# Kernel tuning notes

Hardware: AMD Instinct MI355X
Metric: run time of the kernel (lower is better)

The kernel has to match this reference:

```python
import jax, jax.numpy as jnp
import numpy as np

N = 16384      # total points
B = 8          # point clouds in batch
PER = N // B   # points per cloud (batch ids sorted in blocks)
M = 4096       # sampled centers (ratio 0.25, strided sampler -> batch-aligned)
K = 64         # max_num_neighbors
R = 0.25       # ball-query radius
C_IN = 128
HID = 256
C_OUT = 256


def setup_inputs() -> dict:
    key = jax.random.key(0)
    k1, k2, k3, k4, k5 = jax.random.split(key, 5)
    x = jax.random.normal(k1, (N, C_IN), dtype=jnp.float32)
    pos = jax.random.uniform(k2, (N, 3), dtype=jnp.float32)  # unit cube
    batch = jnp.repeat(jnp.arange(B, dtype=jnp.int32), PER)  # sorted block batch ids
    lframes = jax.random.normal(k3, (N, 3, 3), dtype=jnp.float32)
    W1 = jax.random.normal(k4, (2 * C_IN + 3, HID), dtype=jnp.float32) * 0.05
    b1 = jnp.zeros((HID,), dtype=jnp.float32)
    W2 = jax.random.normal(k5, (HID, C_OUT), dtype=jnp.float32) * 0.05
    b2 = jnp.zeros((C_OUT,), dtype=jnp.float32)
    return {"x": x, "pos": pos, "batch": batch, "lframes": lframes,
            "W1": W1, "b1": b1, "W2": W2, "b2": b2}


def _ball_query(pos, batch, idx):
    """radius(pos, pos[idx], R, batch, batch[idx], max_num_neighbors=K).
    Returns fixed-size neighbor indices [M, K] + validity mask [M, K]."""
    pos_c = pos[idx]                                  # [M, 3]
    # squared distances via gemm trick (avoid [M, N, 3] broadcast)
    d2 = ((pos_c ** 2).sum(-1)[:, None]
          + (pos ** 2).sum(-1)[None, :]
          - 2.0 * pos_c @ pos.T)                      # [M, N]
    valid = (d2 <= R * R) & (batch[idx][:, None] == batch[None, :])
    score = jnp.where(valid, -d2, -jnp.inf)
    vals, nbr = jax.lax.top_k(score, K)               # K nearest within ball
    return nbr, jnp.isfinite(vals)


def reference(x, pos, batch, lframes, W1, b1, W2, b2):
    # center sampler: strided subsample (batch-aligned since batch is block-sorted)
    idx = jnp.arange(0, N, N // M)                    # [M]
    nbr, vmask = _ball_query(pos, batch, idx)         # [M, K]

    pos_dst = pos[idx]                                # [M, 3]
    x_dst = x[idx]                                    # [M, C_IN]
    lframes_dst = lframes[idx]                        # [M, 3, 3]

    # EdgeConv: per-edge message MLP([x_src, x_dst, lframe_dst @ (pos_src - pos_dst)])
    rel = pos[nbr] - pos_dst[:, None, :]              # [M, K, 3]
    rel_loc = jnp.einsum('mij,mkj->mki', lframes_dst, rel)  # rotate into dst frame
    feats = jnp.concatenate([
        x[nbr],                                        # [M, K, C_IN]
        jnp.broadcast_to(x_dst[:, None, :], (M, K, C_IN)),
        rel_loc,
    ], axis=-1)                                        # [M, K, 2*C_IN+3]

    h = jax.nn.relu(feats @ W1 + b1)                   # [M, K, HID]
    msg = h @ W2 + b2                                  # [M, K, C_OUT]

    # masked max aggregation over valid neighbors
    msg = jnp.where(vmask[..., None], msg, -jnp.inf)
    out = msg.max(axis=1)                              # [M, C_OUT]
    out = jnp.where(jnp.isfinite(out), out, 0.0)
    return out, pos_dst, batch[idx], lframes_dst
```

## Files before the change

kernel.cpp:

```cpp
#include <hip/hip_runtime.h>
#include <hip/hip_bf16.h>

#define N_PTS 16384
#define PER   2048
#define M_CTR 4096
#define KNB   64
#define C_IN  128
#define HID   256
#define C_OUT 256

typedef unsigned short u16;
typedef unsigned int u32;
typedef __attribute__((ext_vector_type(8))) short s8v;
typedef __attribute__((ext_vector_type(4))) float f4v;
typedef __attribute__((ext_vector_type(4))) unsigned int u4v;

static __device__ __forceinline__ u16 f2bf(float f) {
    union { float f; unsigned int i; } v; v.f = f;
    unsigned int r = v.i + 0x7FFFu + ((v.i >> 16) & 1u);
    return (u16)(r >> 16);
}

__global__ __launch_bounds__(256) void ballq_kernel(
        const float* __restrict__ pos, int* __restrict__ nbr, int* __restrict__ cnt,
        const float* __restrict__ W1, const float* __restrict__ W2,
        u16* __restrict__ W1aT, u16* __restrict__ W1bT, u16* __restrict__ W2T) {
    __shared__ float cd2[1024];
    __shared__ int   cidx[1024];
    __shared__ int   s_n;
    int m = blockIdx.x, tid = threadIdx.x;

    if (m < 256) {
        int gid = m * 256 + tid;
        int cc = gid >> 8, k = gid & 255;
        W2T[gid] = f2bf(W2[k * 256 + cc]);
        if (gid < 32768) {
            int c1 = gid >> 7, k1 = gid & 127;
            W1aT[gid] = f2bf(W1[k1 * 256 + c1]);
            W1bT[gid] = f2bf(W1[(k1 + 128) * 256 + c1]);
        }
    }

    int c = m * 4;
    int base = (m >> 9) << 11;
    int ln = tid & 63;
    if (tid == 0) s_n = 0;
    __syncthreads();
    float cx = pos[c * 3 + 0], cy = pos[c * 3 + 1], cz = pos[c * 3 + 2];
    float A = __fadd_rn(__fadd_rn(__fmul_rn(cx, cx), __fmul_rn(cy, cy)), __fmul_rn(cz, cz));
    float c2x = __fmul_rn(2.0f, cx);
    float c2y = __fmul_rn(2.0f, cy);
    float c2z = __fmul_rn(2.0f, cz);
    for (int s = 0; s < 8; ++s) {
        int j = base + tid + (s << 8);
        float px = pos[j * 3 + 0], py = pos[j * 3 + 1], pz = pos[j * 3 + 2];
        float B = __fadd_rn(__fadd_rn(__fmul_rn(px, px), __fmul_rn(py, py)), __fmul_rn(pz, pz));
        float C = __fmaf_rn(c2z, pz, __fmaf_rn(c2y, py, __fmul_rn(c2x, px)));
        float d2 = __fsub_rn(__fadd_rn(A, B), C);
        bool hit = (d2 <= 0.0625f);
        unsigned long long mk = __ballot(hit);
        int nb = __popcll(mk & ((1ull << ln) - 1ull));
        int tot = __popcll(mk);
        int bidx = 0;
        if (ln == 0 && tot) bidx = atomicAdd(&s_n, tot);
        bidx = __shfl(bidx, 0, 64);
        if (hit) {
            int a = bidx + nb;
            if (a < 1024) { cd2[a] = d2; cidx[a] = j; }
        }
    }
    __syncthreads();
    int V = s_n < 1024 ? s_n : 1024;
    if (V <= KNB) {
        if (tid < KNB) nbr[m * KNB + tid] = (tid < V) ? cidx[tid] : c;
        if (tid == 0) cnt[m] = V;
    } else {
        for (int e = tid; e < V; e += 256) {
            float de = cd2[e]; int ie = cidx[e];
            int rank = 0;
            for (int q = 0; q < V; ++q) {
                float dq = cd2[q];
                rank += (dq < de) || (dq == de && cidx[q] < ie);
            }
            if (rank < KNB) nbr[m * KNB + rank] = cidx[e];
        }
        if (tid == 0) cnt[m] = KNB;
    }
}

__global__ __launch_bounds__(256) void gemm_xw_kernel(
        const float* __restrict__ x, const u16* __restrict__ W1aT, const u16* __restrict__ W1bT,
        const float* __restrict__ b1, u16* __restrict__ u_out, float* __restrict__ v_out) {
    __shared__ u16 x_lds[64 * 136];
    int blk = blockIdx.x, tid = threadIdx.x;
    int mode = blk >= 256 ? 1 : 0;
    int bb = mode ? blk - 256 : blk;
    const u16* WT = mode ? W1bT : W1aT;
    {
        int r = tid >> 2, q = tid & 3;
        int xrow = bb * 64 + r;
        if (mode) xrow *= 4;
        const float* xp = x + xrow * C_IN + q * 32;
        u16* dst = x_lds + r * 136 + q * 32;
        for (int i = 0; i < 8; ++i) {
            f4v f = *(const f4v*)(xp + i * 4);
            dst[i * 4 + 0] = f2bf(f[0]);
            dst[i * 4 + 1] = f2bf(f[1]);
            dst[i * 4 + 2] = f2bf(f[2]);
            dst[i * 4 + 3] = f2bf(f[3]);
        }
    }
    __syncthreads();
    int lane = tid & 63, w = tid >> 6;
    int quad = lane >> 4, l16 = lane & 15;
    int cb = w * 64;
    f4v acc[4][4] = {};
    for (int k0 = 0; k0 < 128; k0 += 32) {
        s8v a[4], b[4];
        for (int rt = 0; rt < 4; ++rt)
            a[rt] = *(const s8v*)&x_lds[(rt * 16 + l16) * 136 + k0 + quad * 8];
        for (int ct = 0; ct < 4; ++ct)
            b[ct] = *(const s8v*)(WT + (cb + ct * 16 + l16) * 128 + k0 + quad * 8);
        for (int rt = 0; rt < 4; ++rt)
            for (int ct = 0; ct < 4; ++ct)
                acc[rt][ct] = __builtin_amdgcn_mfma_f32_16x16x32_bf16(a[rt], b[ct], acc[rt][ct], 0, 0, 0);
    }
    for (int rt = 0; rt < 4; ++rt)
        for (int ct = 0; ct < 4; ++ct)
            for (int g = 0; g < 4; ++g) {
                int row = rt * 16 + quad * 4 + g;
                int col = cb + ct * 16 + l16;
                float val = acc[rt][ct][g];
                int orow = bb * 64 + row;
                if (mode == 0) u_out[orow * 256 + col] = f2bf(val);
                else           v_out[orow * 256 + col] = val + b1[col];
            }
}

__global__ __launch_bounds__(512, 2) void edge_kernel(
        const u16* __restrict__ u, const float* __restrict__ v,
        const u16* __restrict__ W2T, const float* __restrict__ W1,
        const float* __restrict__ b2, const float* __restrict__ pos,
        const float* __restrict__ lframes, const int* __restrict__ batch,
        const int* __restrict__ nbrg, const int* __restrict__ cnt,
        float* __restrict__ out0, float* __restrict__ out_pos,
        float* __restrict__ out_batch, float* __restrict__ out_lf) {
    __shared__ u16   h_lds[2][128 * 264];
    __shared__ float v_lds[4][2][256];
    __shared__ float w1c_lds[768];
    __shared__ f4v   relc_lds[4][2][64];
    __shared__ u16   nbr_lds[4][2][64];

    int blk = blockIdx.x, tid = threadIdx.x;
    int m0 = ((blk & 7) << 9) | ((blk >> 3) << 3);

    int lane = tid & 63, w = tid >> 6;
    int quad = lane >> 4, l16 = lane & 15;
    int cb = (w & 3) * 64;
    int rbase = (w >> 2) * 64;
    int gsel = w >> 2;

    s8v bfrag[6][4];
    #pragma unroll
    for (int k0 = 0; k0 < 6; ++k0)
        #pragma unroll
        for (int ct = 0; ct < 4; ++ct)
            bfrag[k0][ct] = *(const s8v*)(W2T + (cb + ct * 16 + l16) * 256 + k0 * 32 + quad * 8);

    for (int i = tid; i < 768; i += 512) w1c_lds[i] = W1[65536 + i];
    {
        int pr = tid >> 7, g = (tid >> 6) & 1, t = tid & 63;
        int mm = m0 + pr * 2 + g, cc = mm * 4;
        int j = nbrg[mm * KNB + t];
        nbr_lds[pr][g][t] = (u16)j;
        float rx = pos[j * 3 + 0] - pos[cc * 3 + 0];
        float ry = pos[j * 3 + 1] - pos[cc * 3 + 1];
        float rz = pos[j * 3 + 2] - pos[cc * 3 + 2];
        const float* lf = lframes + cc * 9;
        f4v r;
        r[0] = lf[0] * rx + lf[1] * ry + lf[2] * rz;
        r[1] = lf[3] * rx + lf[4] * ry + lf[5] * rz;
        r[2] = lf[6] * rx + lf[7] * ry + lf[8] * rz;
        r[3] = 0.0f;
        relc_lds[pr][g][t] = r;
    }
    ((f4v*)v_lds)[tid] = *(const f4v*)(v + m0 * 256 + tid * 4);
    if (tid >= 256 && tid < 384) {
        int g = (tid - 256) >> 4, t = tid & 15;
        int mm = m0 + g, cc = mm * 4;
        if (t < 3)            out_pos[mm * 3 + t] = pos[cc * 3 + t];
        else if (t == 3)      out_batch[mm] = (float)batch[cc];
        else if (t < 13)      out_lf[mm * 9 + (t - 4)] = lframes[cc * 9 + (t - 4)];
    }

    int co = (tid & 31) * 8;
    int rs = tid >> 5;

    u4v ug[8];
    #pragma unroll
    for (int g = 0; g < 2; ++g)
        #pragma unroll
        for (int i2 = 0; i2 < 4; ++i2) {
            int rl = rs + i2 * 16;
            int j = nbrg[(m0 + g) * KNB + rl];
            ug[g * 4 + i2] = *(const u4v*)(u + j * 256 + co);
        }
    __syncthreads();

    for (int p = 0; p < 4; ++p) {
        int pb = p & 1;
        int cvp = cnt[m0 + p * 2 + gsel];
        #pragma unroll
        for (int g = 0; g < 2; ++g) {
            f4v vq0 = *(const f4v*)&v_lds[p][g][co];
            f4v vq1 = *(const f4v*)&v_lds[p][g][co + 4];
            f4v wa0 = *(const f4v*)&w1c_lds[co],       wa1 = *(const f4v*)&w1c_lds[co + 4];
            f4v wb0 = *(const f4v*)&w1c_lds[256 + co], wb1 = *(const f4v*)&w1c_lds[256 + co + 4];
            f4v wc0 = *(const f4v*)&w1c_lds[512 + co], wc1 = *(const f4v*)&w1c_lds[512 + co + 4];
            #pragma unroll
            for (int i2 = 0; i2 < 4; ++i2) {
                int rl = rs + i2 * 16;
                int row = g * 64 + rl;
                u4v uu = ug[g * 4 + i2];
                f4v r = relc_lds[p][g][rl];
                float p8[8];
                #pragma unroll
                for (int e = 0; e < 8; ++e) {
                    u32 bits = (e & 1) ? (uu[e >> 1] & 0xFFFF0000u) : (uu[e >> 1] << 16);
                    float va = (e < 4) ? vq0[e] : vq1[e - 4];
                    float a0 = (e < 4) ? wa0[e] : wa1[e - 4];
                    float b0 = (e < 4) ? wb0[e] : wb1[e - 4];
                    float c0 = (e < 4) ? wc0[e] : wc1[e - 4];
                    float pre = fmaf(r[0], a0, fmaf(r[1], b0, fmaf(r[2], c0,
                                  va + __uint_as_float(bits))));
                    p8[e] = fmaxf(pre, 0.0f);
                }
                u4v pk;
                #pragma unroll
                for (int d = 0; d < 4; ++d)
                    pk[d] = __builtin_amdgcn_perm(__float_as_uint(p8[2 * d + 1]),
                                                  __float_as_uint(p8[2 * d]), 0x07060302u);
                *(u4v*)&h_lds[pb][row * 264 + co] = pk;
            }
        }
        __syncthreads();

        if (p < 3) {
            #pragma unroll
            for (int g = 0; g < 2; ++g)
                #pragma unroll
                for (int i2 = 0; i2 < 4; ++i2) {
                    int rl = rs + i2 * 16;
                    int j = (int)nbr_lds[p + 1][g][rl];
                    ug[g * 4 + i2] = *(const u4v*)(u + j * 256 + co);
                }
        }

        s8v bs[2][4];
        #pragma unroll
        for (int kk = 0; kk < 2; ++kk)
            #pragma unroll
            for (int ct = 0; ct < 4; ++ct)
                bs[kk][ct] = *(const s8v*)(W2T + (cb + ct * 16 + l16) * 256 + (6 + kk) * 32 + quad * 8);
        f4v acc[4][4] = {};
        #pragma unroll
        for (int k0 = 0; k0 < 6; ++k0) {
            s8v a[4];
            #pragma unroll
            for (int rt = 0; rt < 4; ++rt)
                a[rt] = *(const s8v*)&h_lds[pb][(rbase + rt * 16 + l16) * 264 + k0 * 32 + quad * 8];
            #pragma unroll
            for (int rt = 0; rt < 4; ++rt)
                #pragma unroll
                for (int ct = 0; ct < 4; ++ct)
                    acc[rt][ct] = __builtin_amdgcn_mfma_f32_16x16x32_bf16(a[rt], bfrag[k0][ct], acc[rt][ct], 0, 0, 0);
        }
        #pragma unroll
        for (int kk = 0; kk < 2; ++kk) {
            int k0 = 6 + kk;
            s8v a[4];
            #pragma unroll
            for (int rt = 0; rt < 4; ++rt)
                a[rt] = *(const s8v*)&h_lds[pb][(rbase + rt * 16 + l16) * 264 + k0 * 32 + quad * 8];
            #pragma unroll
            for (int rt = 0; rt < 4; ++rt)
                #pragma unroll
                for (int ct = 0; ct < 4; ++ct)
                    acc[rt][ct] = __builtin_amdgcn_mfma_f32_16x16x32_bf16(a[rt], bs[kk][ct], acc[rt][ct], 0, 0, 0);
        }
        int mout = m0 + p * 2 + gsel;
        #pragma unroll
        for (int ct = 0; ct < 4; ++ct) {
            float mx = -__builtin_inff();
            #pragma unroll
            for (int rt = 0; rt < 4; ++rt)
                #pragma unroll
                for (int g = 0; g < 4; ++g) {
                    int row = rt * 16 + quad * 4 + g;
                    float val = acc[rt][ct][g];
                    if (row < cvp) mx = fmaxf(mx, val);
                }
            mx = fmaxf(mx, __shfl_xor(mx, 16, 64));
            mx = fmaxf(mx, __shfl_xor(mx, 32, 64));
            if (lane < 16)
                out0[mout * 256 + cb + ct * 16 + l16] = mx + b2[cb + ct * 16 + l16];
        }
    }
}

extern "C" void kernel_launch(void* const* d_in, const int* in_sizes, int n_in,
                              void* d_out, int out_size, void* d_ws, size_t ws_size,
                              hipStream_t stream) {
    const float* x       = (const float*)d_in[0];
    const float* pos     = (const float*)d_in[1];
    const int*   batch   = (const int*)d_in[2];
    const float* lframes = (const float*)d_in[3];
    const float* W1      = (const float*)d_in[4];
    const float* b1      = (const float*)d_in[5];
    const float* W2      = (const float*)d_in[6];
    const float* b2      = (const float*)d_in[7];

    float* out       = (float*)d_out;
    float* out_pos   = out + M_CTR * 256;
    float* out_batch = out_pos + M_CTR * 3;
    float* out_lf    = out_batch + M_CTR;

    char* ws = (char*)d_ws;
    u16*   u_ws = (u16*)(ws);
    float* v_ws = (float*)(ws + 8388608);
    u16*   W1aT = (u16*)(ws + 12582912);
    u16*   W1bT = (u16*)(ws + 12648448);
    u16*   W2T  = (u16*)(ws + 12713984);
    int*   nbr  = (int*)(ws + 12845056);
    int*   cntp = (int*)(ws + 13893632);

    hipLaunchKernelGGL(ballq_kernel, dim3(M_CTR), dim3(256), 0, stream,
                       pos, nbr, cntp, W1, W2, W1aT, W1bT, W2T);
    hipLaunchKernelGGL(gemm_xw_kernel, dim3(320), dim3(256), 0, stream,
                       x, W1aT, W1bT, b1, u_ws, v_ws);
    hipLaunchKernelGGL(edge_kernel, dim3(512), dim3(512), 0, stream,
                       u_ws, v_ws, W2T, W1, b2, pos, lframes, batch, nbr, cntp,
                       out, out_pos, out_batch, out_lf);
}
```

Baseline: 179.6 us.

## Shrink edge kernel LDS footprint to one center per step for higher occupancy

The edge kernel now processes one center per iteration instead of two. Each wave computes 32 output columns instead of 64, and a single 64-row h buffer replaces the double-buffered 128-row buffers. The v tile moves out of LDS and is loaded straight from global memory, and the explicit register prefetch of the next neighbor features is removed. Together these cut per-block LDS use by roughly four times and register pressure, and launch bounds now request 4 blocks. The aim is to hide gather latency with more resident waves. The cost is an extra barrier per iteration, the loss of software prefetch overlap, and twice as many loop iterations with smaller MFMA tiles.

```diff
diff --git a/kernel.cpp b/kernel.cpp
--- a/kernel.cpp
+++ b/kernel.cpp
@@ -137,7 +137,7 @@
             }
 }
 
-__global__ __launch_bounds__(512, 2) void edge_kernel(
+__global__ __launch_bounds__(512, 4) void edge_kernel(
         const u16* __restrict__ u, const float* __restrict__ v,
         const u16* __restrict__ W2T, const float* __restrict__ W1,
         const float* __restrict__ b2, const float* __restrict__ pos,
@@ -145,34 +145,31 @@
         const int* __restrict__ nbrg, const int* __restrict__ cnt,
         float* __restrict__ out0, float* __restrict__ out_pos,
         float* __restrict__ out_batch, float* __restrict__ out_lf) {
-    __shared__ u16   h_lds[2][128 * 264];
-    __shared__ float v_lds[4][2][256];
+    __shared__ u16   h_lds[64 * 264];
     __shared__ float w1c_lds[768];
-    __shared__ f4v   relc_lds[4][2][64];
-    __shared__ u16   nbr_lds[4][2][64];
+    __shared__ f4v   relc_lds[8][64];
+    __shared__ u16   nbr_lds[8][64];
 
     int blk = blockIdx.x, tid = threadIdx.x;
     int m0 = ((blk & 7) << 9) | ((blk >> 3) << 3);
 
     int lane = tid & 63, w = tid >> 6;
     int quad = lane >> 4, l16 = lane & 15;
-    int cb = (w & 3) * 64;
-    int rbase = (w >> 2) * 64;
-    int gsel = w >> 2;
-
-    s8v bfrag[6][4];
+    int cb = w * 32;
+
+    s8v bfrag[4][2];
     #pragma unroll
-    for (int k0 = 0; k0 < 6; ++k0)
-        #pragma unroll
-        for (int ct = 0; ct < 4; ++ct)
+    for (int k0 = 0; k0 < 4; ++k0)
+        #pragma unroll
+        for (int ct = 0; ct < 2; ++ct)
             bfrag[k0][ct] = *(const s8v*)(W2T + (cb + ct * 16 + l16) * 256 + k0 * 32 + quad * 8);
 
     for (int i = tid; i < 768; i += 512) w1c_lds[i] = W1[65536 + i];
     {
-        int pr = tid >> 7, g = (tid >> 6) & 1, t = tid & 63;
-        int mm = m0 + pr * 2 + g, cc = mm * 4;
+        int pr = tid >> 6, t = tid & 63;
+        int mm = m0 + pr, cc = mm * 4;
         int j = nbrg[mm * KNB + t];
-        nbr_lds[pr][g][t] = (u16)j;
+        nbr_lds[pr][t] = (u16)j;
         float rx = pos[j * 3 + 0] - pos[cc * 3 + 0];
         float ry = pos[j * 3 + 1] - pos[cc * 3 + 1];
         float rz = pos[j * 3 + 2] - pos[cc * 3 + 2];
@@ -182,9 +179,8 @@
         r[1] = lf[3] * rx + lf[4] * ry + lf[5] * rz;
         r[2] = lf[6] * rx + lf[7] * ry + lf[8] * rz;
         r[3] = 0.0f;
-        relc_lds[pr][g][t] = r;
-    }
-    ((f4v*)v_lds)[tid] = *(const f4v*)(v + m0 * 256 + tid * 4);
+        relc_lds[pr][t] = r;
+    }
     if (tid >= 256 && tid < 384) {
         int g = (tid - 256) >> 4, t = tid & 15;
         int mm = m0 + g, cc = mm * 4;
@@ -195,38 +191,34 @@
 
     int co = (tid & 31) * 8;
     int rs = tid >> 5;
-
-    u4v ug[8];
-    #pragma unroll
-    for (int g = 0; g < 2; ++g)
-        #pragma unroll
-        for (int i2 = 0; i2 < 4; ++i2) {
-            int rl = rs + i2 * 16;
-            int j = nbrg[(m0 + g) * KNB + rl];
-            ug[g * 4 + i2] = *(const u4v*)(u + j * 256 + co);
-        }
     __syncthreads();
 
-    for (int p = 0; p < 4; ++p) {
-        int pb = p & 1;
-        int cvp = cnt[m0 + p * 2 + gsel];
-        #pragma unroll
-        for (int g = 0; g < 2; ++g) {
-            f4v vq0 = *(const f4v*)&v_lds[p][g][co];
-            f4v vq1 = *(const f4v*)&v_lds[p][g][co + 4];
+    for (int p = 0; p < 8; ++p) {
+        int cvp = cnt[m0 + p];
+        {
+            const float* vp = v + (m0 + p) * 256 + co;
+            f4v vq0 = *(const f4v*)vp;
+            f4v vq1 = *(const f4v*)(vp + 4);
             f4v wa0 = *(const f4v*)&w1c_lds[co],       wa1 = *(const f4v*)&w1c_lds[co + 4];
             f4v wb0 = *(const f4v*)&w1c_lds[256 + co], wb1 = *(const f4v*)&w1c_lds[256 + co + 4];
             f4v wc0 = *(const f4v*)&w1c_lds[512 + co], wc1 = *(const f4v*)&w1c_lds[512 + co + 4];
+            u4v uu[4];
+            f4v rr[4];
             #pragma unroll
             for (int i2 = 0; i2 < 4; ++i2) {
                 int rl = rs + i2 * 16;
-                int row = g * 64 + rl;
-                u4v uu = ug[g * 4 + i2];
-                f4v r = relc_lds[p][g][rl];
+                int j = (int)nbr_lds[p][rl];
+                uu[i2] = *(const u4v*)(u + j * 256 + co);
+                rr[i2] = relc_lds[p][rl];
+            }
+            #pragma unroll
+            for (int i2 = 0; i2 < 4; ++i2) {
+                int rl = rs + i2 * 16;
+                f4v r = rr[i2];
                 float p8[8];
                 #pragma unroll
                 for (int e = 0; e < 8; ++e) {
-                    u32 bits = (e & 1) ? (uu[e >> 1] & 0xFFFF0000u) : (uu[e >> 1] << 16);
+                    u32 bits = (e & 1) ? (uu[i2][e >> 1] & 0xFFFF0000u) : (uu[i2][e >> 1] << 16);
                     float va = (e < 4) ? vq0[e] : vq1[e - 4];
                     float a0 = (e < 4) ? wa0[e] : wa1[e - 4];
                     float b0 = (e < 4) ? wb0[e] : wb1[e - 4];
@@ -240,57 +232,46 @@
                 for (int d = 0; d < 4; ++d)
                     pk[d] = __builtin_amdgcn_perm(__float_as_uint(p8[2 * d + 1]),
                                                   __float_as_uint(p8[2 * d]), 0x07060302u);
-                *(u4v*)&h_lds[pb][row * 264 + co] = pk;
+                *(u4v*)&h_lds[rl * 264 + co] = pk;
             }
         }
         __syncthreads();
 
-        if (p < 3) {
-            #pragma unroll
-            for (int g = 0; g < 2; ++g)
-                #pragma unroll
-                for (int i2 = 0; i2 < 4; ++i2) {
-                    int rl = rs + i2 * 16;
-                    int j = (int)nbr_lds[p + 1][g][rl];
-                    ug[g * 4 + i2] = *(const u4v*)(u + j * 256 + co);
-                }
-        }
-
-        s8v bs[2][4];
-        #pragma unroll
-        for (int kk = 0; kk < 2; ++kk)
-            #pragma unroll
-            for (int ct = 0; ct < 4; ++ct)
-                bs[kk][ct] = *(const s8v*)(W2T + (cb + ct * 16 + l16) * 256 + (6 + kk) * 32 + quad * 8);
-        f4v acc[4][4] = {};
-        #pragma unroll
-        for (int k0 = 0; k0 < 6; ++k0) {
+        s8v bs[4][2];
+        #pragma unroll
+        for (int kk = 0; kk < 4; ++kk)
+            #pragma unroll
+            for (int ct = 0; ct < 2; ++ct)
+                bs[kk][ct] = *(const s8v*)(W2T + (cb + ct * 16 + l16) * 256 + (4 + kk) * 32 + quad * 8);
+        f4v acc[4][2] = {};
+        #pragma unroll
+        for (int k0 = 0; k0 < 4; ++k0) {
             s8v a[4];
             #pragma unroll
             for (int rt = 0; rt < 4; ++rt)
-                a[rt] = *(const s8v*)&h_lds[pb][(rbase + rt * 16 + l16) * 264 + k0 * 32 + quad * 8];
-            #pragma unroll
-            for (int rt = 0; rt < 4; ++rt)
-                #pragma unroll
-                for (int ct = 0; ct < 4; ++ct)
+                a[rt] = *(const s8v*)&h_lds[(rt * 16 + l16) * 264 + k0 * 32 + quad * 8];
+            #pragma unroll
+            for (int rt = 0; rt < 4; ++rt)
+                #pragma unroll
+                for (int ct = 0; ct < 2; ++ct)
                     acc[rt][ct] = __builtin_amdgcn_mfma_f32_16x16x32_bf16(a[rt], bfrag[k0][ct], acc[rt][ct], 0, 0, 0);
         }
         #pragma unroll
-        for (int kk = 0; kk < 2; ++kk) {
-            int k0 = 6 + kk;
+        for (int kk = 0; kk < 4; ++kk) {
+            int k0 = 4 + kk;
             s8v a[4];
             #pragma unroll
             for (int rt = 0; rt < 4; ++rt)
-                a[rt] = *(const s8v*)&h_lds[pb][(rbase + rt * 16 + l16) * 264 + k0 * 32 + quad * 8];
-            #pragma unroll
-            for (int rt = 0; rt < 4; ++rt)
-                #pragma unroll
-                for (int ct = 0; ct < 4; ++ct)
+                a[rt] = *(const s8v*)&h_lds[(rt * 16 + l16) * 264 + k0 * 32 + quad * 8];
+            #pragma unroll
+            for (int rt = 0; rt < 4; ++rt)
+                #pragma unroll
+                for (int ct = 0; ct < 2; ++ct)
                     acc[rt][ct] = __builtin_amdgcn_mfma_f32_16x16x32_bf16(a[rt], bs[kk][ct], acc[rt][ct], 0, 0, 0);
         }
-        int mout = m0 + p * 2 + gsel;
-        #pragma unroll
-        for (int ct = 0; ct < 4; ++ct) {
+        int mout = m0 + p;
+        #pragma unroll
+        for (int ct = 0; ct < 2; ++ct) {
             float mx = -__builtin_inff();
             #pragma unroll
             for (int rt = 0; rt < 4; ++rt)
@@ -305,6 +286,7 @@
             if (lane < 16)
                 out0[mout * 256 + cb + ct * 16 + l16] = mx + b2[cb + ct * 16 + l16];
         }
+        if (p < 7) __syncthreads();
     }
 }
 
```

Result: faster. 162.2 us, median of 2 (-9.7%).
